# Kernel optimization log

Hardware: AMD Instinct MI355X
Metric: run time of the kernel (lower is better)

The kernel has to match this reference:

```python
import math
import jax, jax.numpy as jnp
from jax import lax
import numpy as np

NUM_EXPERTS = 8
TOP_K = 2
CAPACITY_FACTOR = 1.25
AUX_COEF = 0.01


def setup_inputs() -> dict:
    key = jax.random.key(0)
    k1, k2, k3, k4, k5 = jax.random.split(key, 5)
    B, T, C, I, E = 4, 2048, 768, 3072, NUM_EXPERTS
    x = jax.random.normal(k1, (B, T, C), dtype=jnp.float32)
    Wr = jax.random.normal(k2, (C, E), dtype=jnp.float32) * 0.02
    Wg = jax.random.normal(k3, (E, C, I), dtype=jnp.float32) * 0.02
    Wu = jax.random.normal(k4, (E, C, I), dtype=jnp.float32) * 0.02
    Wp = jax.random.normal(k5, (E, I, C), dtype=jnp.float32) * 0.02
    return {"x": x, "Wr": Wr, "Wg": Wg, "Wu": Wu, "Wp": Wp}


def reference(x, Wr, Wg, Wu, Wp):
    E, K = NUM_EXPERTS, TOP_K
    B, T, C = x.shape
    N = B * T
    capacity = max(1, math.ceil(CAPACITY_FACTOR * N / E))  # static: 1280
    xf = x.reshape(N, C)

    # --- router ---
    logits = xf @ Wr                                    # [N, E]
    probs = jax.nn.softmax(logits.astype(jnp.float32), axis=-1)
    gates, idx = lax.top_k(probs, K)                    # [N, 2] each
    gates = gates / jnp.clip(jnp.sum(gates, axis=-1, keepdims=True), 1e-9)

    # --- aux load-balancing loss ---
    oh1 = jax.nn.one_hot(idx[:, 0], E, dtype=jnp.int32)  # [N, E]
    oh2 = jax.nn.one_hot(idx[:, 1], E, dtype=jnp.int32)
    importance = probs.mean(axis=0)
    load = (oh1 + oh2).astype(jnp.float32).mean(axis=0) / K
    aux_loss = jnp.sum(importance * load) * E * AUX_COEF

    # --- capacity positions (running rank within each expert) ---
    pos1 = jnp.sum((jnp.cumsum(oh1, axis=0) - 1) * oh1, axis=-1)   # [N]
    mask1 = pos1 < capacity
    slot1 = idx[:, 0] * capacity + pos1
    count1 = jnp.minimum(jnp.sum(oh1, axis=0), capacity)           # [E]
    pos2 = jnp.sum((jnp.cumsum(oh2, axis=0) - 1) * oh2, axis=-1) + count1[idx[:, 1]]
    mask2 = pos2 < capacity
    slot2 = idx[:, 1] * capacity + pos2

    # --- dispatch (scatter into per-expert buffers; OOB slots dropped) ---
    buf = jnp.zeros((E * capacity, C), dtype=x.dtype)
    s1 = jnp.where(mask1, slot1, E * capacity)
    s2 = jnp.where(mask2, slot2, E * capacity)
    buf = buf.at[s1].set(xf, mode='drop')
    buf = buf.at[s2].set(xf, mode='drop')
    ein = buf.reshape(E, capacity, C)

    # --- per-expert swiglu MLP (grouped GEMMs) ---
    gate = jax.nn.silu(jnp.einsum('enc,ech->enh', ein, Wg))
    up = jnp.einsum('enc,ech->enh', ein, Wu)
    out = jnp.einsum('enh,ehc->enc', gate * up, Wp).reshape(E * capacity, C)

    # --- combine (gather back to token order, renormalized gates) ---
    g1 = gates[:, 0] * mask1.astype(jnp.float32)
    g2 = gates[:, 1] * mask2.astype(jnp.float32)
    denom = jnp.clip(g1 + g2, 1e-9)
    g1 = (g1 / denom).astype(x.dtype)
    g2 = (g2 / denom).astype(x.dtype)
    c1 = jnp.clip(slot1, 0, E * capacity - 1)
    c2 = jnp.clip(slot2, 0, E * capacity - 1)
    y = g1[:, None] * out[c1] + g2[:, None] * out[c2]
    return y.reshape(B, T, C), aux_loss
```

## Files before the change

kernel.cpp:

```cpp
#include <hip/hip_runtime.h>
#include <cstdint>
#include <cstddef>

#define NTOK 8192
#define NEXP 8
#define CAP 1280
#define CDIM 768
#define IDIM 3072
#define EROWS (NEXP*CAP)

typedef __attribute__((ext_vector_type(8))) short short8;
typedef __attribute__((ext_vector_type(4))) float f32x4;
typedef __attribute__((ext_vector_type(4))) unsigned short us4;
typedef __attribute__((ext_vector_type(8))) unsigned short us8;

__device__ __forceinline__ unsigned short f2b(float f) {
  unsigned u = __builtin_bit_cast(unsigned, f);
  u += 0x7FFFu + ((u >> 16) & 1u);
  return (unsigned short)(u >> 16);
}
__device__ __forceinline__ float b2f(unsigned short u) {
  return __builtin_bit_cast(float, ((unsigned)u) << 16);
}

__global__ __launch_bounds__(256) void transpose_cvt64(const float* __restrict__ src,
    unsigned short* __restrict__ dst, int R, int S) {
  int tilesS = S >> 6, tilesR = R >> 6;
  int perE = tilesR * tilesS;
  int e = blockIdx.x / perE;
  int rem = blockIdx.x % perE;
  int rt = rem / tilesS, st = rem % tilesS;
  const float* se = src + (size_t)e*R*S + ((size_t)rt*64)*S + st*64;
  unsigned short* de = dst + (size_t)e*R*S + ((size_t)st*64)*R + rt*64;
  __shared__ float tile[64][65];
  int c4 = (threadIdx.x & 15)*4, rr = threadIdx.x >> 4;
#pragma unroll
  for (int p = 0; p < 4; ++p) {
    float4 v = *(const float4*)(se + (size_t)(rr + 16*p)*S + c4);
    tile[rr + 16*p][c4+0] = v.x; tile[rr + 16*p][c4+1] = v.y;
    tile[rr + 16*p][c4+2] = v.z; tile[rr + 16*p][c4+3] = v.w;
  }
  __syncthreads();
#pragma unroll
  for (int p = 0; p < 4; ++p) {
    int s = rr + 16*p;
    us4 o;
    o.x = f2b(tile[c4+0][s]); o.y = f2b(tile[c4+1][s]);
    o.z = f2b(tile[c4+2][s]); o.w = f2b(tile[c4+3][s]);
    *(us4*)(de + (size_t)s*R + c4) = o;
  }
}

__global__ __launch_bounds__(256) void wgu_cvt64(const float* __restrict__ Wg,
    const float* __restrict__ Wu, unsigned short* __restrict__ Wgu) {
  const int tilesR = CDIM/64, tilesS = IDIM/64;
  const int perE = tilesR * tilesS;
  int sel = blockIdx.x / (NEXP*perE);
  int rem = blockIdx.x % (NEXP*perE);
  int e = rem / perE; int r2 = rem % perE;
  int rt = r2 / tilesS, st = r2 % tilesS;
  const float* se = (sel ? Wu : Wg) + (size_t)e*CDIM*IDIM + ((size_t)rt*64)*IDIM + st*64;
  __shared__ float tile[64][65];
  int c4 = (threadIdx.x & 15)*4, rr = threadIdx.x >> 4;
#pragma unroll
  for (int p = 0; p < 4; ++p) {
    float4 v = *(const float4*)(se + (size_t)(rr + 16*p)*IDIM + c4);
    tile[rr + 16*p][c4+0] = v.x; tile[rr + 16*p][c4+1] = v.y;
    tile[rr + 16*p][c4+2] = v.z; tile[rr + 16*p][c4+3] = v.w;
  }
  __syncthreads();
  unsigned short* dstE = Wgu + (size_t)e*(2*IDIM)*CDIM;
#pragma unroll
  for (int p = 0; p < 4; ++p) {
    int s = rr + 16*p;
    int np = 128*st + 32*(s>>4) + (s&15) + sel*16;
    us4 o;
    o.x = f2b(tile[c4+0][s]); o.y = f2b(tile[c4+1][s]);
    o.z = f2b(tile[c4+2][s]); o.w = f2b(tile[c4+3][s]);
    *(us4*)(dstE + (size_t)np*CDIM + rt*64 + c4) = o;
  }
}

__global__ __launch_bounds__(256) void router_kernel(const float* __restrict__ x,
    const float* __restrict__ Wr, float* __restrict__ probs,
    int* __restrict__ idx1, int* __restrict__ idx2,
    float* __restrict__ g1r, float* __restrict__ g2r) {
  __shared__ float WrT[NEXP*CDIM];
  for (int i = threadIdx.x; i < NEXP*CDIM; i += 256) {
    int c = i >> 3, e = i & 7;
    WrT[e*CDIM + c] = Wr[i];
  }
  __syncthreads();
  int w = threadIdx.x >> 6, l = threadIdx.x & 63;
  int t = blockIdx.x*4 + w;
  float acc[NEXP];
#pragma unroll
  for (int e = 0; e < NEXP; ++e) acc[e] = 0.f;
  for (int k = 0; k < CDIM/64; ++k) {
    float xv = x[(size_t)t*CDIM + k*64 + l];
#pragma unroll
    for (int e = 0; e < NEXP; ++e) acc[e] += xv * WrT[e*CDIM + k*64 + l];
  }
#pragma unroll
  for (int off = 32; off > 0; off >>= 1) {
#pragma unroll
    for (int e = 0; e < NEXP; ++e) acc[e] += __shfl_xor(acc[e], off);
  }
  if (l == 0) {
    float m = acc[0];
#pragma unroll
    for (int e = 1; e < NEXP; ++e) m = fmaxf(m, acc[e]);
    float p[NEXP]; float s = 0.f;
#pragma unroll
    for (int e = 0; e < NEXP; ++e) { p[e] = expf(acc[e] - m); s += p[e]; }
    float inv = 1.f / s;
#pragma unroll
    for (int e = 0; e < NEXP; ++e) { p[e] *= inv; probs[(size_t)t*NEXP + e] = p[e]; }
    int i1 = 0; float b1 = p[0];
#pragma unroll
    for (int e = 1; e < NEXP; ++e) if (p[e] > b1) { b1 = p[e]; i1 = e; }
    int i2 = -1; float b2 = -1e30f;
#pragma unroll
    for (int e = 0; e < NEXP; ++e) if (e != i1 && p[e] > b2) { b2 = p[e]; i2 = e; }
    float gs = fmaxf(b1 + b2, 1e-9f);
    g1r[t] = b1 / gs; g2r[t] = b2 / gs;
    idx1[t] = i1; idx2[t] = i2;
  }
}

__global__ __launch_bounds__(1024) void scan_kernel(
    const int* __restrict__ idx1, const int* __restrict__ idx2,
    const float* __restrict__ g1r, const float* __restrict__ g2r,
    const float* __restrict__ probs,
    int* __restrict__ bufmap,
    int* __restrict__ c1o, int* __restrict__ c2o,
    float* __restrict__ g1o, float* __restrict__ g2o,
    float* __restrict__ aux_out) {
  __shared__ unsigned int scanbuf[1024][9];
  __shared__ unsigned int totals[NEXP];
  int tid = threadIdx.x;
  int e1[8], e2[8];
  unsigned int cnt[NEXP];
#pragma unroll
  for (int k = 0; k < NEXP; ++k) cnt[k] = 0;
  for (int j = 0; j < 8; ++j) {
    int t = tid*8 + j;
    e1[j] = idx1[t]; e2[j] = idx2[t];
    cnt[e1[j]] += 1u;
    cnt[e2[j]] += (1u << 16);
  }
#pragma unroll
  for (int k = 0; k < NEXP; ++k) scanbuf[tid][k] = cnt[k];
  unsigned int run[NEXP];
#pragma unroll
  for (int k = 0; k < NEXP; ++k) run[k] = cnt[k];
  __syncthreads();
  for (int off = 1; off < 1024; off <<= 1) {
    unsigned int add[NEXP];
#pragma unroll
    for (int k = 0; k < NEXP; ++k) add[k] = 0;
    if (tid >= off) {
#pragma unroll
      for (int k = 0; k < NEXP; ++k) add[k] = scanbuf[tid - off][k];
    }
    __syncthreads();
#pragma unroll
    for (int k = 0; k < NEXP; ++k) { run[k] += add[k]; scanbuf[tid][k] = run[k]; }
    __syncthreads();
  }
  if (tid == 1023) {
#pragma unroll
    for (int k = 0; k < NEXP; ++k) totals[k] = run[k];
  }
  __syncthreads();
  unsigned int excl[NEXP];
#pragma unroll
  for (int k = 0; k < NEXP; ++k) excl[k] = run[k] - cnt[k];
  int cnt1c[NEXP];
#pragma unroll
  for (int k = 0; k < NEXP; ++k) cnt1c[k] = min((int)(totals[k] & 0xFFFFu), CAP);

  for (int j = 0; j < 8; ++j) {
    int t = tid*8 + j;
    int a = e1[j];
    int pos1 = (int)(excl[a] & 0xFFFFu); excl[a] += 1u;
    int slot1 = a*CAP + pos1;
    bool m1 = pos1 < CAP;
    if (m1) bufmap[slot1] = t;
    int b = e2[j];
    int pos2 = (int)(excl[b] >> 16) + cnt1c[b]; excl[b] += (1u << 16);
    int slot2 = b*CAP + pos2;
    bool m2 = pos2 < CAP;
    if (m2) bufmap[slot2] = t;
    float G1 = m1 ? g1r[t] : 0.f;
    float G2 = m2 ? g2r[t] : 0.f;
    float den = fmaxf(G1 + G2, 1e-9f);
    g1o[t] = G1 / den; g2o[t] = G2 / den;
    c1o[t] = min(slot1, EROWS - 1);
    c2o[t] = min(slot2, EROWS - 1);
  }

  float imp[NEXP];
#pragma unroll
  for (int k = 0; k < NEXP; ++k) imp[k] = 0.f;
  for (int j = 0; j < 8; ++j) {
    int t = tid*8 + j;
    const float4* pr = (const float4*)(probs + (size_t)t*NEXP);
    float4 a0 = pr[0], a1 = pr[1];
    imp[0] += a0.x; imp[1] += a0.y; imp[2] += a0.z; imp[3] += a0.w;
    imp[4] += a1.x; imp[5] += a1.y; imp[6] += a1.z; imp[7] += a1.w;
  }
  __syncthreads();
  float* fbuf = (float*)&scanbuf[0][0];
#pragma unroll
  for (int k = 0; k < NEXP; ++k) fbuf[tid*9 + k] = imp[k];
  __syncthreads();
  for (int s = 512; s >= 1; s >>= 1) {
    if (tid < s) {
#pragma unroll
      for (int k = 0; k < NEXP; ++k) fbuf[tid*9 + k] += fbuf[(tid + s)*9 + k];
    }
    __syncthreads();
  }
  if (tid == 0) {
    float aux = 0.f;
#pragma unroll
    for (int k = 0; k < NEXP; ++k) {
      float importance = fbuf[k] / (float)NTOK;
      float loadk = (float)((totals[k] & 0xFFFFu) + (totals[k] >> 16)) / ((float)NTOK * 2.0f);
      aux += importance * loadk;
    }
    aux_out[0] = aux * (float)NEXP * 0.01f;
  }
}

__global__ __launch_bounds__(192) void dispatch_kernel(const float* __restrict__ x,
    const int* __restrict__ bufmap, unsigned short* __restrict__ ein) {
  int r = blockIdx.x;
  int t = bufmap[r];
  int q = threadIdx.x;
  float4 v = make_float4(0.f, 0.f, 0.f, 0.f);
  if (t >= 0) v = ((const float4*)x)[(size_t)t*(CDIM/4) + q];
  us4 o;
  o.x = f2b(v.x); o.y = f2b(v.y); o.z = f2b(v.z); o.w = f2b(v.w);
  ((us4*)ein)[(size_t)r*(CDIM/4) + q] = o;
}

#define BAR  asm volatile("s_barrier" ::: "memory")
#define VMW(N) asm volatile("s_waitcnt vmcnt(" #N ")" ::: "memory")
#define P1 __builtin_amdgcn_s_setprio(1)
#define P0 __builtin_amdgcn_s_setprio(0)

template<int KD>
__global__ __launch_bounds__(512, 2) void gemm1_8ph(
    const unsigned short* __restrict__ A,
    const unsigned short* __restrict__ Bw,
    unsigned short* __restrict__ H) {
  constexpr int NT = KD/64;
  constexpr int NITER = NT/2;
  __shared__ unsigned short lds[81920];

  const int bid = blockIdx.x;
  const int chunk = gridDim.x >> 3;
  const int tile = (bid & 7)*chunk + (bid >> 3);
  const int e = tile / 120;
  const int rem = tile % 120;
  const int nt = rem / 5, mt = rem % 5;

  const int tid = threadIdx.x;
  const int l = tid & 63, wid = tid >> 6;
  const int wr = wid >> 2, wc = wid & 3;
  const int lrow = l & 15, khi = l >> 4;

  const unsigned short* Ab = A  + (size_t)e*CAP*KD      + (size_t)mt*256*KD;
  const unsigned short* Bb = Bw + (size_t)e*(2*IDIM)*KD + (size_t)nt*256*KD;

  const int srow = tid >> 3;
  const int scol = (tid & 7) ^ (srow & 7);
  const size_t lane_off = (size_t)srow*KD + scol*8;
  const int lds_st = wid*512;

#define STG(dstu, srcp, half, kt) do { \
    const unsigned short* s_ = (srcp) + lane_off + (size_t)(half)*128*KD + (size_t)(kt)*64; \
    unsigned short* d_ = (unsigned short*)lds + (dstu) + (half)*8192 + lds_st; \
    __builtin_amdgcn_global_load_lds((const __attribute__((address_space(1))) void*)s_, \
        (__attribute__((address_space(3))) void*)d_, 16, 0, 0); \
    __builtin_amdgcn_global_load_lds((const __attribute__((address_space(1))) void*)(s_ + (size_t)64*KD), \
        (__attribute__((address_space(3))) void*)(d_ + 4096), 16, 0, 0); \
  } while(0)

  const int swz0 = ((khi    ) ^ (lrow & 7)) * 8;
  const int swz1 = ((4 + khi) ^ (lrow & 7)) * 8;
  const int aoff = wr*8192 + lrow*64;
  const int boff = (wc>>1)*8192 + ((wc&1)*64 + lrow)*64;

#define LDA(ab, dst, mb) do { _Pragma("unroll") for (int m_=0;m_<4;++m_) { \
    dst[m_][0] = *(const short8*)(lds + (ab) + aoff + ((mb)+m_)*1024 + swz0); \
    dst[m_][1] = *(const short8*)(lds + (ab) + aoff + ((mb)+m_)*1024 + swz1); } } while(0)
#define LDB(bb, dst, nb) do { _Pragma("unroll") for (int n_=0;n_<2;++n_) { \
    dst[n_][0] = *(const short8*)(lds + (bb) + boff + ((nb)+n_)*1024 + swz0); \
    dst[n_][1] = *(const short8*)(lds + (bb) + boff + ((nb)+n_)*1024 + swz1); } } while(0)
#define QUAD(af, bf, mb, nb) do { _Pragma("unroll") for (int r_=0;r_<2;++r_) \
    _Pragma("unroll") for (int n_=0;n_<2;++n_) \
    _Pragma("unroll") for (int m_=0;m_<4;++m_) \
      acc[(mb)+m_][(nb)+n_] = __builtin_amdgcn_mfma_f32_16x16x32_bf16(af[m_][r_], bf[n_][r_], acc[(mb)+m_][(nb)+n_], 0,0,0); } while(0)

  f32x4 acc[8][4];
#pragma unroll
  for (int i = 0; i < 8; ++i)
#pragma unroll
    for (int j = 0; j < 4; ++j) acc[i][j] = (f32x4){0.f,0.f,0.f,0.f};

  short8 a[4][2], bl[2][2], bh[2][2];

  int bA_ = 32768, bB_ = 49152, bC_ = 65536;

  STG(0, Ab, 0, 0);      STG(bA_, Bb, 0, 0);
  STG(0, Ab, 1, 0);      STG(bA_, Bb, 1, 0);
  STG(16384, Ab, 0, 1);  STG(bB_, Bb, 0, 1);
  STG(16384, Ab, 1, 1);  STG(bB_, Bb, 1, 1);
  VMW(8);
  BAR;

#define ITER(t2, t3, DOS, VM4, VM8) \
    LDA(0, a, 0); LDB(bA_, bl, 0); if (DOS) STG(bC_, Bb, 0, (t2)); \
    BAR; P1; QUAD(a, bl, 0, 0); P0; BAR; \
    LDB(bA_, bh, 2); if (DOS) STG(bC_, Bb, 1, (t2)); \
    BAR; P1; QUAD(a, bh, 0, 2); P0; BAR; \
    LDA(0, a, 4); \
    BAR; P1; QUAD(a, bh, 4, 2); P0; BAR; \
    if (DOS) STG(0, Ab, 0, (t2)); VM4; \
    BAR; P1; QUAD(a, bl, 4, 0); P0; BAR; \
    LDA(16384, a, 0); LDB(bB_, bl, 0); if (DOS) { STG(0, Ab, 1, (t2)); STG(bA_, Bb, 0, (t3)); } \
    BAR; P1; QUAD(a, bl, 0, 0); P0; BAR; \
    LDB(bB_, bh, 2); if (DOS) STG(bA_, Bb, 1, (t3)); \
    BAR; P1; QUAD(a, bh, 0, 2); P0; BAR; \
    LDA(16384, a, 4); \
    BAR; P1; QUAD(a, bh, 4, 2); P0; BAR; \
    if (DOS) { STG(16384, Ab, 0, (t3)); STG(16384, Ab, 1, (t3)); } VM8; \
    BAR; P1; QUAD(a, bl, 4, 0); P0; BAR;

#pragma unroll 1
  for (int i = 0; i < NITER-1; ++i) {
    const int t2 = 2*i+2, t3 = 2*i+3;
    ITER(t2, t3, true, VMW(6), VMW(8));
    int tmp = bC_; bC_ = bB_; bB_ = bA_; bA_ = tmp;
  }
  ITER(0, 0, false, VMW(0), VMW(0));

#undef ITER
#undef QUAD
#undef LDB
#undef LDA
#undef STG

  __syncthreads();
  {
    const int cb0 = wc*32 + lrow;
    const int rb0 = wr*128 + khi*4;
#pragma unroll
    for (int m = 0; m < 8; ++m)
#pragma unroll
      for (int p = 0; p < 2; ++p) {
        f32x4 g = acc[m][2*p], u = acc[m][2*p+1];
#pragma unroll
        for (int r = 0; r < 4; ++r) {
          float gv = g[r];
          float hv = gv / (1.f + __expf(-gv)) * u[r];
          lds[(rb0 + m*16 + r)*136 + cb0 + p*16] = f2b(hv);
        }
      }
  }
  __syncthreads();
  const size_t rowg = (size_t)e*CAP + (size_t)mt*256;
  const size_t colg = (size_t)nt*128 + (size_t)(l & 15)*8;
#pragma unroll
  for (int i = 0; i < 8; ++i) {
    int row = wid*32 + i*4 + (l >> 4);
    us8 v = *(const us8*)(lds + row*136 + (l & 15)*8);
    *(us8*)(H + (rowg + row)*(size_t)IDIM + colg) = v;
  }
}

template<int K>
__global__ __launch_bounds__(256, 2) void gemm_bt(
    const unsigned short* __restrict__ A,
    const unsigned short* __restrict__ B0,
    unsigned short* __restrict__ Fout,
    int Ntiles, int N) {
  constexpr int MT = 10;
  int chunk = gridDim.x >> 3;
  int bid = blockIdx.x;
  int tile = (bid & 7)*chunk + (bid >> 3);
  int perE = MT * Ntiles;
  int e = tile / perE, rem = tile % perE;
  int mt = rem / Ntiles, nt = rem % Ntiles;

  const unsigned short* Ae  = A  + (size_t)e*CAP*K + (size_t)mt*128*K;
  const unsigned short* B0e = B0 + (size_t)e*N*K   + (size_t)nt*128*K;

  __shared__ unsigned short sh[16384];
  unsigned short* Alds = sh;
  unsigned short* B0lds = sh + 8192;

  int tid = threadIdx.x;
  int l = tid & 63, w = tid >> 6;
  int rbase = w*8 + (l >> 3);
  int csrc  = (l & 7) ^ ((l >> 3) & 7);
  size_t gbase = (size_t)rbase*K + (size_t)csrc*8;
  int ldsoff = w*512;

  f32x4 acc0[16];
#pragma unroll
  for (int i = 0; i < 16; ++i) acc0[i] = (f32x4){0.f,0.f,0.f,0.f};

  int wm = (w >> 1)*64, wn = (w & 1)*64;
  int lrow = l & 15, khi = l >> 4;

  for (int kt = 0; kt < K/64; ++kt) {
    const unsigned short* Ag  = Ae  + gbase + (size_t)kt*64;
    const unsigned short* Bg0 = B0e + gbase + (size_t)kt*64;
#pragma unroll
    for (int q = 0; q < 4; ++q) {
      __builtin_amdgcn_global_load_lds(
          (const __attribute__((address_space(1))) void*)(Ag + (size_t)q*32*K),
          (__attribute__((address_space(3))) void*)(Alds + ldsoff + q*2048), 16, 0, 0);
    }
#pragma unroll
    for (int q = 0; q < 4; ++q) {
      __builtin_amdgcn_global_load_lds(
          (const __attribute__((address_space(1))) void*)(Bg0 + (size_t)q*32*K),
          (__attribute__((address_space(3))) void*)(B0lds + ldsoff + q*2048), 16, 0, 0);
    }
    __syncthreads();
#pragma unroll
    for (int kk = 0; kk < 2; ++kk) {
      int cs = (kk*4 + khi) ^ (l & 7);
      short8 af[4];
#pragma unroll
      for (int m = 0; m < 4; ++m) {
        int row = wm + m*16 + lrow;
        af[m] = *(const short8*)(Alds + row*64 + cs*8);
      }
#pragma unroll
      for (int n = 0; n < 4; ++n) {
        int rowb = wn + n*16 + lrow;
        short8 b0 = *(const short8*)(B0lds + rowb*64 + cs*8);
#pragma unroll
        for (int m = 0; m < 4; ++m)
          acc0[m*4+n] = __builtin_amdgcn_mfma_f32_16x16x32_bf16(af[m], b0, acc0[m*4+n], 0, 0, 0);
      }
    }
    __syncthreads();
  }

  const size_t rowg = (size_t)e*CAP + (size_t)mt*128;
  const size_t colg = (size_t)nt*128;
#pragma unroll
  for (int h = 0; h < 2; ++h) {
    if ((w >> 1) == h) {
#pragma unroll
      for (int m = 0; m < 4; ++m)
#pragma unroll
        for (int n = 0; n < 4; ++n) {
          f32x4 v = acc0[m*4+n];
#pragma unroll
          for (int r = 0; r < 4; ++r)
            sh[(m*16 + khi*4 + r)*136 + wn + n*16 + lrow] = f2b(v[r]);
        }
    }
    __syncthreads();
#pragma unroll
    for (int jj = 0; jj < 4; ++jj) {
      int idx = tid + 256*jj;
      int rp = idx >> 4, ch = idx & 15;
      us8 v = *(const us8*)(sh + rp*136 + ch*8);
      *(us8*)(Fout + (rowg + h*64 + rp)*(size_t)N + colg + ch*8) = v;
    }
    __syncthreads();
  }
}

__global__ __launch_bounds__(192) void combine_kernel(const unsigned short* __restrict__ outbuf,
    const int* __restrict__ c1, const int* __restrict__ c2,
    const float* __restrict__ g1, const float* __restrict__ g2,
    float* __restrict__ y) {
  int t = blockIdx.x;
  int q = threadIdx.x;
  float f1 = g1[t], f2 = g2[t];
  int a = c1[t], b = c2[t];
  us4 va = ((const us4*)outbuf)[(size_t)a*(CDIM/4) + q];
  us4 vb = ((const us4*)outbuf)[(size_t)b*(CDIM/4) + q];
  float4 r;
  r.x = f1*b2f(va.x) + f2*b2f(vb.x);
  r.y = f1*b2f(va.y) + f2*b2f(vb.y);
  r.z = f1*b2f(va.z) + f2*b2f(vb.z);
  r.w = f1*b2f(va.w) + f2*b2f(vb.w);
  ((float4*)y)[(size_t)t*(CDIM/4) + q] = r;
}

extern "C" void kernel_launch(void* const* d_in, const int* in_sizes, int n_in,
                              void* d_out, int out_size, void* d_ws, size_t ws_size,
                              hipStream_t stream) {
  const float* x  = (const float*)d_in[0];
  const float* Wr = (const float*)d_in[1];
  const float* Wg = (const float*)d_in[2];
  const float* Wu = (const float*)d_in[3];
  const float* Wp = (const float*)d_in[4];
  float* y = (float*)d_out;

  char* p = (char*)d_ws;
  auto alloc = [&](size_t bytes) { char* r = p; p += (bytes + 255) & ~(size_t)255; return r; };
  unsigned short* WguT = (unsigned short*)alloc((size_t)NEXP*2*IDIM*CDIM*2);
  unsigned short* WpT  = (unsigned short*)alloc((size_t)NEXP*CDIM*IDIM*2);
  unsigned short* ein  = (unsigned short*)alloc((size_t)EROWS*CDIM*2);
  unsigned short* h    = (unsigned short*)alloc((size_t)EROWS*IDIM*2);
  unsigned short* outbuf = (unsigned short*)alloc((size_t)EROWS*CDIM*2);
  float* probs  = (float*)alloc((size_t)NTOK*NEXP*4);
  int* idx1 = (int*)alloc(NTOK*4);
  int* idx2 = (int*)alloc(NTOK*4);
  int* c1   = (int*)alloc(NTOK*4);
  int* c2   = (int*)alloc(NTOK*4);
  float* g1r = (float*)alloc(NTOK*4);
  float* g2r = (float*)alloc(NTOK*4);
  float* g1o = (float*)alloc(NTOK*4);
  float* g2o = (float*)alloc(NTOK*4);
  int* bufmap = (int*)alloc(EROWS*4);

  size_t required = (size_t)(p - (char*)d_ws);
  if (ws_size < required) return;

  hipMemsetAsync(bufmap, 0xFF, EROWS*sizeof(int), stream);

  wgu_cvt64<<<2*NEXP*(CDIM/64)*(IDIM/64), 256, 0, stream>>>(Wg, Wu, WguT);
  transpose_cvt64<<<NEXP*(IDIM/64)*(CDIM/64), 256, 0, stream>>>(Wp, WpT, IDIM, CDIM);

  router_kernel<<<NTOK/4, 256, 0, stream>>>(x, Wr, probs, idx1, idx2, g1r, g2r);
  scan_kernel<<<1, 1024, 0, stream>>>(idx1, idx2, g1r, g2r, probs, bufmap,
                                      c1, c2, g1o, g2o, y + (size_t)NTOK*CDIM);
  dispatch_kernel<<<EROWS, 192, 0, stream>>>(x, bufmap, ein);

  gemm1_8ph<CDIM><<<NEXP*5*(2*IDIM/256), 512, 0, stream>>>(ein, WguT, h);
  gemm_bt<IDIM><<<NEXP*10*(CDIM/128), 256, 0, stream>>>(
      h, WpT, outbuf, CDIM/128, CDIM);

  combine_kernel<<<NTOK, 192, 0, stream>>>(outbuf, c1, c2, g1o, g2o, y);
}
```

Baseline: 312.8 us.

## Replace down-projection GEMM with 8-phase pipelined 256x128 tile kernel

Replaces the simple single-buffered down-projection GEMM (128x128 tiles, 256 threads, a load then sync per k-step) with a 512-thread kernel. It uses 256x128 tiles and triple-buffered B / double-buffered A staging in LDS, reusing the 8-phase schedule, priority hints and vmcnt waits from the first GEMM. The aim is to overlap global-to-LDS loads with MFMA work and raise data reuse per tile. The cost is a large LDS footprint (about 112KB) and fewer blocks (240 instead of 480), which may leave CUs underused on a 256-CU part.

Measured after the change: 295.2 us. -5.6%, faster.

```diff
diff --git a/kernel.cpp b/kernel.cpp
--- a/kernel.cpp
+++ b/kernel.cpp
@@ -349,10 +349,6 @@
   ITER(0, 0, false, VMW(0), VMW(0));
 
 #undef ITER
-#undef QUAD
-#undef LDB
-#undef LDA
-#undef STG
 
   __syncthreads();
   {
@@ -380,104 +376,127 @@
     us8 v = *(const us8*)(lds + row*136 + (l & 15)*8);
     *(us8*)(H + (rowg + row)*(size_t)IDIM + colg) = v;
   }
-}
-
-template<int K>
-__global__ __launch_bounds__(256, 2) void gemm_bt(
+#undef QUAD
+#undef LDB
+#undef LDA
+#undef STG
+}
+
+template<int KD>
+__global__ __launch_bounds__(512, 2) void gemm2_8ph(
     const unsigned short* __restrict__ A,
-    const unsigned short* __restrict__ B0,
-    unsigned short* __restrict__ Fout,
-    int Ntiles, int N) {
-  constexpr int MT = 10;
-  int chunk = gridDim.x >> 3;
-  int bid = blockIdx.x;
-  int tile = (bid & 7)*chunk + (bid >> 3);
-  int perE = MT * Ntiles;
-  int e = tile / perE, rem = tile % perE;
-  int mt = rem / Ntiles, nt = rem % Ntiles;
-
-  const unsigned short* Ae  = A  + (size_t)e*CAP*K + (size_t)mt*128*K;
-  const unsigned short* B0e = B0 + (size_t)e*N*K   + (size_t)nt*128*K;
-
-  __shared__ unsigned short sh[16384];
-  unsigned short* Alds = sh;
-  unsigned short* B0lds = sh + 8192;
-
-  int tid = threadIdx.x;
-  int l = tid & 63, w = tid >> 6;
-  int rbase = w*8 + (l >> 3);
-  int csrc  = (l & 7) ^ ((l >> 3) & 7);
-  size_t gbase = (size_t)rbase*K + (size_t)csrc*8;
-  int ldsoff = w*512;
-
-  f32x4 acc0[16];
-#pragma unroll
-  for (int i = 0; i < 16; ++i) acc0[i] = (f32x4){0.f,0.f,0.f,0.f};
-
-  int wm = (w >> 1)*64, wn = (w & 1)*64;
-  int lrow = l & 15, khi = l >> 4;
-
-  for (int kt = 0; kt < K/64; ++kt) {
-    const unsigned short* Ag  = Ae  + gbase + (size_t)kt*64;
-    const unsigned short* Bg0 = B0e + gbase + (size_t)kt*64;
-#pragma unroll
-    for (int q = 0; q < 4; ++q) {
-      __builtin_amdgcn_global_load_lds(
-          (const __attribute__((address_space(1))) void*)(Ag + (size_t)q*32*K),
-          (__attribute__((address_space(3))) void*)(Alds + ldsoff + q*2048), 16, 0, 0);
-    }
-#pragma unroll
-    for (int q = 0; q < 4; ++q) {
-      __builtin_amdgcn_global_load_lds(
-          (const __attribute__((address_space(1))) void*)(Bg0 + (size_t)q*32*K),
-          (__attribute__((address_space(3))) void*)(B0lds + ldsoff + q*2048), 16, 0, 0);
-    }
-    __syncthreads();
-#pragma unroll
-    for (int kk = 0; kk < 2; ++kk) {
-      int cs = (kk*4 + khi) ^ (l & 7);
-      short8 af[4];
-#pragma unroll
-      for (int m = 0; m < 4; ++m) {
-        int row = wm + m*16 + lrow;
-        af[m] = *(const short8*)(Alds + row*64 + cs*8);
+    const unsigned short* __restrict__ Bw,
+    unsigned short* __restrict__ O) {
+  constexpr int NT = KD/64;
+  constexpr int NITER = NT/2;
+  __shared__ unsigned short lds[57344];
+
+  const int bid = blockIdx.x;
+  const int chunk = gridDim.x >> 3;
+  const int tile = (bid & 7)*chunk + (bid >> 3);
+  const int e = tile / 30;
+  const int rem = tile % 30;
+  const int nt = rem / 5, mt = rem % 5;
+
+  const int tid = threadIdx.x;
+  const int l = tid & 63, wid = tid >> 6;
+  const int wr = wid >> 1, wc = wid & 1;
+  const int lrow = l & 15, khi = l >> 4;
+
+  const unsigned short* Ab = A  + (size_t)e*CAP*KD  + (size_t)mt*256*KD;
+  const unsigned short* Bb = Bw + (size_t)e*CDIM*KD + (size_t)nt*128*KD;
+
+  const int srow = tid >> 3;
+  const int scol = (tid & 7) ^ (srow & 7);
+  const size_t lane_off = (size_t)srow*KD + scol*8;
+  const int lds_st = wid*512;
+
+#define STG(dstu, srcp, half, kt) do { \
+    const unsigned short* s_ = (srcp) + lane_off + (size_t)(half)*128*KD + (size_t)(kt)*64; \
+    unsigned short* d_ = (unsigned short*)lds + (dstu) + (half)*8192 + lds_st; \
+    __builtin_amdgcn_global_load_lds((const __attribute__((address_space(1))) void*)s_, \
+        (__attribute__((address_space(3))) void*)d_, 16, 0, 0); \
+    __builtin_amdgcn_global_load_lds((const __attribute__((address_space(1))) void*)(s_ + (size_t)64*KD), \
+        (__attribute__((address_space(3))) void*)(d_ + 4096), 16, 0, 0); \
+  } while(0)
+
+  const int swz0 = ((khi    ) ^ (lrow & 7)) * 8;
+  const int swz1 = ((4 + khi) ^ (lrow & 7)) * 8;
+  const int aoff = wr*4096 + lrow*64;
+  const int boff = wc*4096 + lrow*64;
+
+#define LDA(ab, dst) do { _Pragma("unroll") for (int m_=0;m_<4;++m_) { \
+    dst[m_][0] = *(const short8*)(lds + (ab) + aoff + m_*1024 + swz0); \
+    dst[m_][1] = *(const short8*)(lds + (ab) + aoff + m_*1024 + swz1); } } while(0)
+#define LDB(bb, dst, nb) do { _Pragma("unroll") for (int n_=0;n_<2;++n_) { \
+    dst[n_][0] = *(const short8*)(lds + (bb) + boff + ((nb)+n_)*1024 + swz0); \
+    dst[n_][1] = *(const short8*)(lds + (bb) + boff + ((nb)+n_)*1024 + swz1); } } while(0)
+#define QUAD(af, bf, nb) do { _Pragma("unroll") for (int r_=0;r_<2;++r_) \
+    _Pragma("unroll") for (int n_=0;n_<2;++n_) \
+    _Pragma("unroll") for (int m_=0;m_<4;++m_) \
+      acc[m_][(nb)+n_] = __builtin_amdgcn_mfma_f32_16x16x32_bf16(af[m_][r_], bf[n_][r_], acc[m_][(nb)+n_], 0,0,0); } while(0)
+
+  f32x4 acc[4][4];
+#pragma unroll
+  for (int i = 0; i < 4; ++i)
+#pragma unroll
+    for (int j = 0; j < 4; ++j) acc[i][j] = (f32x4){0.f,0.f,0.f,0.f};
+
+  short8 a[4][2], bl[2][2], bh[2][2];
+
+  int bA_ = 32768, bB_ = 40960, bC_ = 49152;
+
+  STG(0, Ab, 0, 0); STG(0, Ab, 1, 0); STG(bA_, Bb, 0, 0);
+  STG(16384, Ab, 0, 1); STG(16384, Ab, 1, 1); STG(bB_, Bb, 0, 1);
+  VMW(6);
+  BAR;
+
+#define ITER2(t2, t3, DOS, VM2, VM4) \
+    LDA(0, a); LDB(bA_, bl, 0); if (DOS) STG(bC_, Bb, 0, (t2)); \
+    BAR; P1; QUAD(a, bl, 0); P0; BAR; \
+    LDB(bA_, bh, 2); if (DOS) { STG(0, Ab, 0, (t2)); STG(0, Ab, 1, (t2)); } VM2; \
+    BAR; P1; QUAD(a, bh, 2); P0; BAR; \
+    LDA(16384, a); LDB(bB_, bl, 0); if (DOS) STG(bA_, Bb, 0, (t3)); \
+    BAR; P1; QUAD(a, bl, 0); P0; BAR; \
+    LDB(bB_, bh, 2); if (DOS) { STG(16384, Ab, 0, (t3)); STG(16384, Ab, 1, (t3)); } VM4; \
+    BAR; P1; QUAD(a, bh, 2); P0; BAR;
+
+#pragma unroll 1
+  for (int i = 0; i < NITER-1; ++i) {
+    const int t2 = 2*i+2, t3 = 2*i+3;
+    ITER2(t2, t3, true, VMW(6), VMW(6));
+    int tmp = bC_; bC_ = bB_; bB_ = bA_; bA_ = tmp;
+  }
+  ITER2(0, 0, false, VMW(0), VMW(0));
+
+#undef ITER2
+#undef QUAD
+#undef LDB
+#undef LDA
+#undef STG
+
+  __syncthreads();
+  {
+    const int cb0 = wc*64 + lrow;
+    const int rb0 = wr*64 + khi*4;
+#pragma unroll
+    for (int m = 0; m < 4; ++m)
+#pragma unroll
+      for (int n = 0; n < 4; ++n) {
+        f32x4 v = acc[m][n];
+#pragma unroll
+        for (int r = 0; r < 4; ++r)
+          lds[(rb0 + m*16 + r)*136 + cb0 + n*16] = f2b(v[r]);
       }
-#pragma unroll
-      for (int n = 0; n < 4; ++n) {
-        int rowb = wn + n*16 + lrow;
-        short8 b0 = *(const short8*)(B0lds + rowb*64 + cs*8);
-#pragma unroll
-        for (int m = 0; m < 4; ++m)
-          acc0[m*4+n] = __builtin_amdgcn_mfma_f32_16x16x32_bf16(af[m], b0, acc0[m*4+n], 0, 0, 0);
-      }
-    }
-    __syncthreads();
-  }
-
-  const size_t rowg = (size_t)e*CAP + (size_t)mt*128;
-  const size_t colg = (size_t)nt*128;
-#pragma unroll
-  for (int h = 0; h < 2; ++h) {
-    if ((w >> 1) == h) {
-#pragma unroll
-      for (int m = 0; m < 4; ++m)
-#pragma unroll
-        for (int n = 0; n < 4; ++n) {
-          f32x4 v = acc0[m*4+n];
-#pragma unroll
-          for (int r = 0; r < 4; ++r)
-            sh[(m*16 + khi*4 + r)*136 + wn + n*16 + lrow] = f2b(v[r]);
-        }
-    }
-    __syncthreads();
-#pragma unroll
-    for (int jj = 0; jj < 4; ++jj) {
-      int idx = tid + 256*jj;
-      int rp = idx >> 4, ch = idx & 15;
-      us8 v = *(const us8*)(sh + rp*136 + ch*8);
-      *(us8*)(Fout + (rowg + h*64 + rp)*(size_t)N + colg + ch*8) = v;
-    }
-    __syncthreads();
+  }
+  __syncthreads();
+  const size_t rowg = (size_t)e*CAP + (size_t)mt*256;
+  const size_t colg = (size_t)nt*128 + (size_t)(l & 15)*8;
+#pragma unroll
+  for (int i = 0; i < 8; ++i) {
+    int row = wid*32 + i*4 + (l >> 4);
+    us8 v = *(const us8*)(lds + row*136 + (l & 15)*8);
+    *(us8*)(O + (rowg + row)*(size_t)CDIM + colg) = v;
   }
 }
 
@@ -541,8 +560,7 @@
   dispatch_kernel<<<EROWS, 192, 0, stream>>>(x, bufmap, ein);
 
   gemm1_8ph<CDIM><<<NEXP*5*(2*IDIM/256), 512, 0, stream>>>(ein, WguT, h);
-  gemm_bt<IDIM><<<NEXP*10*(CDIM/128), 256, 0, stream>>>(
-      h, WpT, outbuf, CDIM/128, CDIM);
+  gemm2_8ph<IDIM><<<NEXP*5*(CDIM/128), 512, 0, stream>>>(h, WpT, outbuf);
 
   combine_kernel<<<NTOK, 192, 0, stream>>>(outbuf, c1, c2, g1o, g2o, y);
 }
```
